# Kernel optimization log

Hardware: AMD Instinct MI355X
Metric: run time of the kernel (lower is better)

Reference implementation:

```python
import jax, jax.numpy as jnp
import numpy as np

B, DV, W, H = 128, 2048, 14, 14
S = W * H            # 196 spatial positions
DQ = 2048            # question vector dim
DA = 1200            # attention dim_v == dim_q == dim_mm (MLB elementwise fusion)
G = 4                # nb_glimpses
DH = 2048            # fusion dim_h (total); per-glimpse = DH // G
NANS = 3000


def setup_inputs() -> dict:
    key = jax.random.key(0)
    ks = jax.random.split(key, 16)
    s = 0.02
    return {
        "input_v": jax.random.normal(ks[0], (B, DV, W, H), jnp.float32),
        "x_q_vec": jax.random.normal(ks[1], (B, DQ), jnp.float32),
        # conv_v_att: 1x1 conv DV->DA  (expressed as channel matmul)
        "Wv_att": jax.random.normal(ks[2], (DV, DA), jnp.float32) * s,
        "bv_att": jnp.zeros((DA,), jnp.float32),
        # linear_q_att: DQ->DA
        "Wq_att": jax.random.normal(ks[3], (DQ, DA), jnp.float32) * s,
        "bq_att": jnp.zeros((DA,), jnp.float32),
        # conv_att: 1x1 conv DA->G
        "Wa": jax.random.normal(ks[4], (DA, G), jnp.float32) * s,
        "ba": jnp.zeros((G,), jnp.float32),
        # per-glimpse fusion linears DV -> DH//G, stacked over glimpses
        "Wf": jax.random.normal(ks[5], (G, DV, DH // G), jnp.float32) * s,
        "bf": jnp.zeros((G, DH // G), jnp.float32),
        # linear_q_fusion: DQ -> DH
        "Wqf": jax.random.normal(ks[6], (DQ, DH), jnp.float32) * s,
        "bqf": jnp.zeros((DH,), jnp.float32),
        # linear_classif: DH -> NANS
        "Wc": jax.random.normal(ks[7], (DH, NANS), jnp.float32) * s,
        "bc": jnp.zeros((NANS,), jnp.float32),
    }


def reference(input_v, x_q_vec, Wv_att, bv_att, Wq_att, bq_att, Wa, ba,
              Wf, bf, Wqf, bqf, Wc, bc):
    b = input_v.shape[0]
    v_flat = input_v.reshape(b, DV, S)                      # [B, DV, S]

    # --- attention scores ---
    # conv_v_att (1x1) + tanh -> [B, S, DA]
    x_v = jnp.tanh(jnp.einsum('bcs,cd->bsd', v_flat, Wv_att) + bv_att)
    # linear_q_att + tanh -> [B, DA], broadcast over spatial
    x_q = jnp.tanh(x_q_vec @ Wq_att + bq_att)
    # MLB fusion_att: elementwise multiply, then tanh (activation_mm)
    x_att = jnp.tanh(x_v * x_q[:, None, :])                 # [B, S, DA]
    scores = jnp.einsum('bsd,dg->bsg', x_att, Wa) + ba      # [B, S, G]
    att = jax.nn.softmax(scores, axis=1)                    # softmax over spatial

    # --- weighted pooling per glimpse ---
    v_att = jnp.einsum('bsg,bcs->bgc', att, v_flat)         # [B, G, DV]

    # --- fusion of glimpses ---
    xv = jnp.tanh(jnp.einsum('bgc,gch->bgh', v_att, Wf) + bf)  # [B, G, DH/G]
    xv = xv.reshape(b, DH)                                   # concat glimpses
    xq = jnp.tanh(x_q_vec @ Wqf + bqf)                       # [B, DH]
    x = xv * xq                                              # MLB fusion_classif

    # --- classifier ---
    x = jnp.tanh(x)
    return x @ Wc + bc                                       # [B, NANS]
```

## Files before the change

kernel.cpp:

```cpp
#include <hip/hip_runtime.h>
#include <hip/hip_bf16.h>

#define BB   128
#define DV   2048
#define SS   196
#define DQ   2048
#define DA   1200
#define DAP  1280
#define GG   4
#define DH   2048
#define NANS 3000
#define NANSP 3008
#define MROWS (BB*SS)
#define NT   10
#define KSPLIT 8
#define KCHUNK (DV/KSPLIT)
#define NQ   (DAP + DH)

typedef __attribute__((ext_vector_type(8))) short bf16x8;
typedef __attribute__((ext_vector_type(4))) float f32x4;

__device__ __forceinline__ float fast_tanh(float x) {
    float e = __expf(2.0f * x);
    return 1.0f - 2.0f * __builtin_amdgcn_rcpf(e + 1.0f);
}

__device__ __forceinline__ void async_copy16(const void* gsrc, void* ldst) {
    __builtin_amdgcn_global_load_lds(
        (const __attribute__((address_space(1))) void*)gsrc,
        (__attribute__((address_space(3))) void*)ldst, 16, 0, 0);
}

__global__ void pad_misc(const float* __restrict__ bv, const float* __restrict__ Wa,
                         float* __restrict__ bvp, float* __restrict__ wap) {
    int i = blockIdx.x * 256 + threadIdx.x;
    if (i < DAP) bvp[i] = (i < DA) ? bv[i] : 0.f;
    if (i < DAP * GG) {
        int d = i >> 2;
        wap[i] = (d < DA) ? Wa[i] : 0.f;
    }
}

__global__ __launch_bounds__(256) void transpose_v(const float* __restrict__ v,
                                                   __hip_bfloat16* __restrict__ vt) {
    __shared__ float tile[128][65];
    const int b  = blockIdx.z;
    const int c0 = blockIdx.x * 128;
    const int s0 = blockIdx.y * 64;
    const int t  = threadIdx.x;
    const int sl = t & 63;
    const int cr = t >> 6;
    const float* src = v + (size_t)b * DV * SS;
    const int sg = s0 + sl;
    const bool sok = sg < SS;
#pragma unroll
    for (int i = 0; i < 32; ++i) {
        int c = cr + i * 4;
        tile[c][sl] = sok ? src[(size_t)(c0 + c) * SS + sg] : 0.f;
    }
    __syncthreads();
    const int cp = (t & 63) * 2;
#pragma unroll
    for (int i = 0; i < 16; ++i) {
        int s = (t >> 6) + i * 4;
        int sgl = s0 + s;
        if (sgl < SS) {
            __hip_bfloat162 h2;
            h2.x = __float2bfloat16(tile[cp][s]);
            h2.y = __float2bfloat16(tile[cp + 1][s]);
            *(__hip_bfloat162*)(vt + ((size_t)b * SS + sgl) * DV + c0 + cp) = h2;
        }
    }
}

__global__ __launch_bounds__(256) void transpose_w(const float* __restrict__ Wv,
                                                   __hip_bfloat16* __restrict__ wvt) {
    __shared__ float tile[64][65];
    const int d0 = blockIdx.x * 64;
    const int c0 = blockIdx.y * 64;
    const int t  = threadIdx.x;
    const int col  = t & 63;
    const int rowb = t >> 6;
#pragma unroll
    for (int i = 0; i < 16; ++i) {
        int c = rowb + i * 4;
        int d = d0 + col;
        tile[c][col] = (d < DA) ? Wv[(size_t)(c0 + c) * DA + d] : 0.f;
    }
    __syncthreads();
#pragma unroll
    for (int i = 0; i < 16; ++i) {
        int dl = rowb + i * 4;
        wvt[(size_t)(d0 + dl) * DV + c0 + col] = __float2bfloat16(tile[col][dl]);
    }
}

template <int SEL>
__global__ __launch_bounds__(256) void gemm_partial(
    const float* __restrict__ A, int lda,
    const float* __restrict__ Bm, const float* __restrict__ B2,
    float* __restrict__ Cp, int Npad) {
    __shared__ float As[64 * 132];
    __shared__ float Bs[64 * 68];
    const int t     = threadIdx.x;
    const int n0    = blockIdx.x * 64;
    const int kbase = blockIdx.y * KCHUNK;

    const float* Aeff = A;
    const float* Beff;
    int ldb, ncol0, nlim;
    if (SEL == 0) {
        Beff = Bm; ldb = NANS; ncol0 = n0; nlim = NANS;
    } else if (SEL == 1) {
        int gg = n0 >> 9;
        Aeff = A + gg * 2048;
        Beff = Bm + (size_t)gg * 2048 * 512;
        ldb = 512; ncol0 = n0 & 511; nlim = 1 << 30;
    } else {
        if (n0 < DAP) { Beff = Bm; ldb = DA; ncol0 = n0;      nlim = DA; }
        else          { Beff = B2; ldb = DH; ncol0 = n0 - DAP; nlim = 1 << 30; }
    }

    const int tm = (t & 31) * 4;
    const int tn = (t >> 5) * 8;
    float acc[4][8] = {};

    for (int k0 = kbase; k0 < kbase + KCHUNK; k0 += 64) {
        {
            int kk = t & 63, mb = (t >> 6) * 32;
#pragma unroll
            for (int i = 0; i < 32; ++i)
                As[kk * 132 + mb + i] = Aeff[(size_t)(mb + i) * lda + k0 + kk];
        }
        {
            int j = t & 63, kr = t >> 6;
            bool ok = (ncol0 + j) < nlim;
#pragma unroll
            for (int i = 0; i < 16; ++i) {
                int k = kr + i * 4;
                Bs[k * 68 + j] = ok ? Beff[(size_t)(k0 + k) * ldb + ncol0 + j] : 0.f;
            }
        }
        __syncthreads();
#pragma unroll
        for (int kk = 0; kk < 64; ++kk) {
            const float4 av = *(const float4*)(As + kk * 132 + tm);
            const float4 b0 = *(const float4*)(Bs + kk * 68 + tn);
            const float4 b1 = *(const float4*)(Bs + kk * 68 + tn + 4);
            const float am[4] = {av.x, av.y, av.z, av.w};
#pragma unroll
            for (int i = 0; i < 4; ++i) {
                acc[i][0] += am[i] * b0.x; acc[i][1] += am[i] * b0.y;
                acc[i][2] += am[i] * b0.z; acc[i][3] += am[i] * b0.w;
                acc[i][4] += am[i] * b1.x; acc[i][5] += am[i] * b1.y;
                acc[i][6] += am[i] * b1.z; acc[i][7] += am[i] * b1.w;
            }
        }
        __syncthreads();
    }
#pragma unroll
    for (int i = 0; i < 4; ++i) {
        size_t base = ((size_t)blockIdx.y * 128 + tm + i) * Npad + n0 + tn;
        float4 v0 = {acc[i][0], acc[i][1], acc[i][2], acc[i][3]};
        float4 v1 = {acc[i][4], acc[i][5], acc[i][6], acc[i][7]};
        *(float4*)(Cp + base) = v0;
        *(float4*)(Cp + base + 4) = v1;
    }
}

template <int MODE>
__global__ __launch_bounds__(256) void gemm_epilogue(
    const float* __restrict__ Cp, int Npad, int Nreal,
    const float* __restrict__ bias, const float* __restrict__ aux,
    float* __restrict__ out, int ldo) {
    int n = blockIdx.x * 256 + threadIdx.x;
    int m = blockIdx.y;
    if (n >= Npad) return;
    float s = 0.f;
#pragma unroll
    for (int ks = 0; ks < KSPLIT; ++ks)
        s += Cp[((size_t)ks * 128 + m) * Npad + n];
    if (MODE == 0) {
        if (n >= Nreal) return;
        out[(size_t)m * ldo + n] = s + bias[n];
    } else {
        float xv = fast_tanh(s + bias[n]);
        out[(size_t)m * ldo + n] = fast_tanh(xv * aux[(size_t)m * 2048 + n]);
    }
}

__global__ __launch_bounds__(256) void epilogue_q(
    const float* __restrict__ Cp,
    const float* __restrict__ bqa, const float* __restrict__ bqf,
    float* __restrict__ qatt, float* __restrict__ qfus) {
    int n = blockIdx.x * 256 + threadIdx.x;
    int m = blockIdx.y;
    if (n >= NQ) return;
    float s = 0.f;
#pragma unroll
    for (int ks = 0; ks < KSPLIT; ++ks)
        s += Cp[((size_t)ks * 128 + m) * NQ + n];
    if (n < DAP) {
        qatt[(size_t)m * DAP + n] = (n < DA) ? fast_tanh(s + bqa[n]) : 0.f;
    } else {
        int j = n - DAP;
        qfus[(size_t)m * DH + j] = fast_tanh(s + bqf[j]);
    }
}

__global__ __launch_bounds__(256) void big_gemm(
    const __hip_bfloat16* __restrict__ vt,
    const __hip_bfloat16* __restrict__ wt,
    const float* __restrict__ bvp,
    const float* __restrict__ qatt,
    const float* __restrict__ wap,
    float* __restrict__ scores_p) {
    __shared__ __hip_bfloat16 As[128 * 64];
    __shared__ __hip_bfloat16 Bs[128 * 64];
    __shared__ float wa_s[128 * 4];
    __shared__ float sc[128 * 4];
    __shared__ float qs[2 * 128];
    const int t    = threadIdx.x;
    const int lane = t & 63;
    const int w    = t >> 6;
    const int wm   = w >> 1, wn = w & 1;

    int bid = blockIdx.x;
    int grp = bid / 80, r = bid % 80;
    int mt, nt;
    if (grp < 24) { mt = grp * 8 + (r & 7); nt = r >> 3; }
    else          { mt = 192 + (r & 3);     nt = r >> 2; }
    const int m0 = mt * 128, n0 = nt * 128;
    const int b0 = m0 / SS;
    const int b1 = (m0 + 127) / SS;
    const int bsplit = (b0 + 1) * SS;

    if (t < 128) {
        *(float4*)(wa_s + t * 4) = *(const float4*)(wap + (n0 + t) * 4);
        *(float4*)(sc + t * 4) = (float4){0.f, 0.f, 0.f, 0.f};
        qs[t]       = qatt[(size_t)b0 * DAP + n0 + t];
        qs[128 + t] = qatt[(size_t)b1 * DAP + n0 + t];
    }

    f32x4 acc[4][4];
#pragma unroll
    for (int i = 0; i < 4; ++i)
#pragma unroll
        for (int j = 0; j < 4; ++j) acc[i][j] = (f32x4){0.f, 0.f, 0.f, 0.f};

    const int srow   = lane >> 3;
    const int schunk = (lane & 7) ^ srow;
    const __hip_bfloat16* aG = vt + (size_t)(m0 + w * 32 + srow) * DV + schunk * 8;
    const __hip_bfloat16* bG = wt + (size_t)(n0 + w * 32 + srow) * DV + schunk * 8;
    __hip_bfloat16* aL = As + (w * 32) * 64;
    __hip_bfloat16* bL = Bs + (w * 32) * 64;

    for (int k0 = 0; k0 < DV; k0 += 64) {
        __syncthreads();
#pragma unroll
        for (int j = 0; j < 4; ++j) {
            async_copy16(aG + (size_t)(j * 8) * DV + k0, aL + j * 8 * 64);
            async_copy16(bG + (size_t)(j * 8) * DV + k0, bL + j * 8 * 64);
        }
        __syncthreads();
#pragma unroll
        for (int ks = 0; ks < 2; ++ks) {
            const int cx = ((ks * 4 + (lane >> 4)) ^ (lane & 7)) * 8;
            bf16x8 a[4], b[4];
#pragma unroll
            for (int mi = 0; mi < 4; ++mi)
                a[mi] = *(const bf16x8*)(As + (wm * 64 + mi * 16 + (lane & 15)) * 64 + cx);
#pragma unroll
            for (int ni = 0; ni < 4; ++ni)
                b[ni] = *(const bf16x8*)(Bs + (wn * 64 + ni * 16 + (lane & 15)) * 64 + cx);
#pragma unroll
            for (int mi = 0; mi < 4; ++mi)
#pragma unroll
                for (int ni = 0; ni < 4; ++ni)
                    acc[mi][ni] = __builtin_amdgcn_mfma_f32_16x16x32_bf16(a[mi], b[ni], acc[mi][ni], 0, 0, 0);
        }
    }

    const int colb_l = wn * 64 + (lane & 15);
    const int colb_g = n0 + colb_l;
    float bvv[4];
    float4 wv[4];
#pragma unroll
    for (int ni = 0; ni < 4; ++ni) {
        bvv[ni] = bvp[colb_g + ni * 16];
        wv[ni]  = *(const float4*)(wa_s + (colb_l + ni * 16) * 4);
    }
#pragma unroll
    for (int mi = 0; mi < 4; ++mi) {
#pragma unroll
        for (int rr = 0; rr < 4; ++rr) {
            int lrow = wm * 64 + mi * 16 + ((lane >> 4) << 2) + rr;
            int row  = m0 + lrow;
            int qoff = (row >= bsplit) ? 128 : 0;
            float p0 = 0.f, p1 = 0.f, p2 = 0.f, p3 = 0.f;
#pragma unroll
            for (int ni = 0; ni < 4; ++ni) {
                float xv = fast_tanh(acc[mi][ni][rr] + bvv[ni]);
                float xa = fast_tanh(xv * qs[qoff + colb_l + ni * 16]);
                p0 += xa * wv[ni].x; p1 += xa * wv[ni].y;
                p2 += xa * wv[ni].z; p3 += xa * wv[ni].w;
            }
#pragma unroll
            for (int mk = 1; mk < 16; mk <<= 1) {
                p0 += __shfl_xor(p0, mk); p1 += __shfl_xor(p1, mk);
                p2 += __shfl_xor(p2, mk); p3 += __shfl_xor(p3, mk);
            }
            if ((lane & 15) == 0) {
                atomicAdd(sc + lrow * 4 + 0, p0);
                atomicAdd(sc + lrow * 4 + 1, p1);
                atomicAdd(sc + lrow * 4 + 2, p2);
                atomicAdd(sc + lrow * 4 + 3, p3);
            }
        }
    }
    __syncthreads();
    if (t < 128)
        *(float4*)(scores_p + ((size_t)nt * MROWS + m0 + t) * 4) = *(float4*)(sc + t * 4);
}

__global__ __launch_bounds__(256) void softmax_pool(
    const float* __restrict__ scores_p,
    const __hip_bfloat16* __restrict__ vt,
    float* __restrict__ vatt) {
    __shared__ __align__(16) float att[SS * GG];
    const int b = blockIdx.y;
    const int t = threadIdx.x;
    if (t < SS) {
        float4 s = {0.f, 0.f, 0.f, 0.f};
#pragma unroll
        for (int ntile = 0; ntile < NT; ++ntile) {
            float4 p = *(const float4*)(scores_p + ((size_t)ntile * MROWS + b * SS + t) * 4);
            s.x += p.x; s.y += p.y; s.z += p.z; s.w += p.w;
        }
        *(float4*)(att + t * 4) = s;
    }
    __syncthreads();
    {
        const int g = t >> 6;
        const int lane = t & 63;
        float mx = -3.0e38f;
        for (int s = lane; s < SS; s += 64) mx = fmaxf(mx, att[s * 4 + g]);
#pragma unroll
        for (int m = 32; m > 0; m >>= 1) mx = fmaxf(mx, __shfl_xor(mx, m));
        float sum = 0.f;
        for (int s = lane; s < SS; s += 64) sum += __expf(att[s * 4 + g] - mx);
#pragma unroll
        for (int m = 32; m > 0; m >>= 1) sum += __shfl_xor(sum, m);
        float inv = __builtin_amdgcn_rcpf(sum);
        for (int s = lane; s < SS; s += 64) att[s * 4 + g] = __expf(att[s * 4 + g] - mx) * inv;
    }
    __syncthreads();
    const int c = blockIdx.x * 512 + t * 2;
    const __hip_bfloat16* vp = vt + (size_t)b * SS * DV + c;
    float a00 = 0, a01 = 0, a02 = 0, a03 = 0;
    float a10 = 0, a11 = 0, a12 = 0, a13 = 0;
#pragma unroll 4
    for (int s = 0; s < SS; ++s) {
        unsigned u = *(const unsigned*)(vp + (size_t)s * DV);
        float v0 = __uint_as_float(u << 16);
        float v1 = __uint_as_float(u & 0xffff0000u);
        float4 aw = *(const float4*)(att + s * 4);
        a00 += v0 * aw.x; a01 += v0 * aw.y; a02 += v0 * aw.z; a03 += v0 * aw.w;
        a10 += v1 * aw.x; a11 += v1 * aw.y; a12 += v1 * aw.z; a13 += v1 * aw.w;
    }
    float* vb = vatt + (size_t)b * GG * DV;
    vb[0 * DV + c] = a00; vb[0 * DV + c + 1] = a10;
    vb[1 * DV + c] = a01; vb[1 * DV + c + 1] = a11;
    vb[2 * DV + c] = a02; vb[2 * DV + c + 1] = a12;
    vb[3 * DV + c] = a03; vb[3 * DV + c + 1] = a13;
}

extern "C" void kernel_launch(void* const* d_in, const int* in_sizes, int n_in,
                              void* d_out, int out_size, void* d_ws, size_t ws_size,
                              hipStream_t stream) {
    const float* input_v = (const float*)d_in[0];
    const float* x_q     = (const float*)d_in[1];
    const float* Wv      = (const float*)d_in[2];
    const float* bv      = (const float*)d_in[3];
    const float* Wq_att  = (const float*)d_in[4];
    const float* bq_att  = (const float*)d_in[5];
    const float* Wa      = (const float*)d_in[6];
    const float* Wf      = (const float*)d_in[8];
    const float* bf_     = (const float*)d_in[9];
    const float* Wqf     = (const float*)d_in[10];
    const float* bqf     = (const float*)d_in[11];
    const float* Wc      = (const float*)d_in[12];
    const float* bc      = (const float*)d_in[13];
    float* out = (float*)d_out;

    char* wsb = (char*)d_ws;
    size_t off = 0;
    auto carve = [&](size_t bytes) -> void* {
        void* p = wsb + off;
        off += (bytes + 255) & ~(size_t)255;
        return p;
    };
    __hip_bfloat16* vt  = (__hip_bfloat16*)carve((size_t)MROWS * DV * 2);
    __hip_bfloat16* wvt = (__hip_bfloat16*)carve((size_t)DAP * DV * 2);
    float* Cp       = (float*)carve((size_t)KSPLIT * 128 * NQ * 4);
    float* scores_p = (float*)carve((size_t)NT * MROWS * GG * 4);
    float* qatt = (float*)carve((size_t)BB * DAP * 4);
    float* qfus = (float*)carve((size_t)BB * DH * 4);
    float* bvp  = (float*)carve((size_t)DAP * 4);
    float* wap  = (float*)carve((size_t)DAP * GG * 4);
    float* vatt = (float*)carve((size_t)BB * GG * DV * 4);
    float* xbuf = (float*)carve((size_t)BB * DH * 4);
    (void)ws_size; (void)n_in; (void)in_sizes; (void)out_size;

    pad_misc<<<dim3(20), 256, 0, stream>>>(bv, Wa, bvp, wap);
    transpose_v<<<dim3(DV / 128, 4, BB), 256, 0, stream>>>(input_v, vt);
    transpose_w<<<dim3(DAP / 64, DV / 64), 256, 0, stream>>>(Wv, wvt);

    gemm_partial<2><<<dim3(NQ / 64, KSPLIT), 256, 0, stream>>>(
        x_q, DQ, Wq_att, Wqf, Cp, NQ);
    epilogue_q<<<dim3(NQ / 256, BB), 256, 0, stream>>>(Cp, bq_att, bqf, qatt, qfus);

    big_gemm<<<dim3(24 * 80 + 40), 256, 0, stream>>>(vt, wvt, bvp, qatt, wap, scores_p);

    softmax_pool<<<dim3(4, BB), 256, 0, stream>>>(scores_p, vt, vatt);

    gemm_partial<1><<<dim3(DH / 64, KSPLIT), 256, 0, stream>>>(
        vatt, GG * DV, Wf, nullptr, Cp, DH);
    gemm_epilogue<2><<<dim3(DH / 256, BB), 256, 0, stream>>>(
        Cp, DH, DH, bf_, qfus, xbuf, DH);

    gemm_partial<0><<<dim3(NANSP / 64, KSPLIT), 256, 0, stream>>>(
        xbuf, DH, Wc, nullptr, Cp, NANSP);
    gemm_epilogue<0><<<dim3(NANSP / 256 + 1, BB), 256, 0, stream>>>(
        Cp, NANSP, NANS, bc, nullptr, out, NANS);
}
```

Baseline: 777.3 us.

## Move small GEMMs to bf16 MFMA split-K and load big_gemm B operand directly to registers

After: 879.2 us. +13.1%, slower.

```diff
diff --git a/kernel.cpp b/kernel.cpp
--- a/kernel.cpp
+++ b/kernel.cpp
@@ -10,12 +10,12 @@
 #define GG   4
 #define DH   2048
 #define NANS 3000
-#define NANSP 3008
+#define NANSP 3072
 #define MROWS (BB*SS)
 #define NT   10
-#define KSPLIT 8
-#define KCHUNK (DV/KSPLIT)
 #define NQ   (DAP + DH)
+#define KS2  16
+#define KCH2 (DV/KS2)
 
 typedef __attribute__((ext_vector_type(8))) short bf16x8;
 typedef __attribute__((ext_vector_type(4))) float f32x4;
@@ -31,9 +31,14 @@
         (__attribute__((address_space(3))) void*)ldst, 16, 0, 0);
 }
 
-__global__ void pad_misc(const float* __restrict__ bv, const float* __restrict__ Wa,
-                         float* __restrict__ bvp, float* __restrict__ wap) {
+__global__ __launch_bounds__(256) void prep(const float* __restrict__ x_q,
+                                            const float* __restrict__ bv,
+                                            const float* __restrict__ Wa,
+                                            __hip_bfloat16* __restrict__ xqb,
+                                            float* __restrict__ bvp,
+                                            float* __restrict__ wap) {
     int i = blockIdx.x * 256 + threadIdx.x;
+    if (i < BB * DQ) xqb[i] = __float2bfloat16(x_q[i]);
     if (i < DAP) bvp[i] = (i < DA) ? bv[i] : 0.f;
     if (i < DAP * GG) {
         int d = i >> 2;
@@ -73,10 +78,13 @@
     }
 }
 
-__global__ __launch_bounds__(256) void transpose_w(const float* __restrict__ Wv,
-                                                   __hip_bfloat16* __restrict__ wvt) {
+__global__ __launch_bounds__(256) void transpose_nk(
+    const float* __restrict__ src, int ldsrc, int nreal,
+    __hip_bfloat16* __restrict__ dst, size_t srcz, int dstzrows) {
+    src += (size_t)blockIdx.z * srcz;
+    dst += (size_t)blockIdx.z * dstzrows * 2048;
     __shared__ float tile[64][65];
-    const int d0 = blockIdx.x * 64;
+    const int n0 = blockIdx.x * 64;
     const int c0 = blockIdx.y * 64;
     const int t  = threadIdx.x;
     const int col  = t & 63;
@@ -84,109 +92,78 @@
 #pragma unroll
     for (int i = 0; i < 16; ++i) {
         int c = rowb + i * 4;
-        int d = d0 + col;
-        tile[c][col] = (d < DA) ? Wv[(size_t)(c0 + c) * DA + d] : 0.f;
+        int n = n0 + col;
+        tile[c][col] = (n < nreal) ? src[(size_t)(c0 + c) * ldsrc + n] : 0.f;
     }
     __syncthreads();
 #pragma unroll
     for (int i = 0; i < 16; ++i) {
-        int dl = rowb + i * 4;
-        wvt[(size_t)(d0 + dl) * DV + c0 + col] = __float2bfloat16(tile[col][dl]);
-    }
-}
-
-template <int SEL>
-__global__ __launch_bounds__(256) void gemm_partial(
-    const float* __restrict__ A, int lda,
-    const float* __restrict__ Bm, const float* __restrict__ B2,
-    float* __restrict__ Cp, int Npad) {
-    __shared__ float As[64 * 132];
-    __shared__ float Bs[64 * 68];
-    const int t     = threadIdx.x;
-    const int n0    = blockIdx.x * 64;
-    const int kbase = blockIdx.y * KCHUNK;
-
-    const float* Aeff = A;
-    const float* Beff;
-    int ldb, ncol0, nlim;
-    if (SEL == 0) {
-        Beff = Bm; ldb = NANS; ncol0 = n0; nlim = NANS;
-    } else if (SEL == 1) {
-        int gg = n0 >> 9;
-        Aeff = A + gg * 2048;
-        Beff = Bm + (size_t)gg * 2048 * 512;
-        ldb = 512; ncol0 = n0 & 511; nlim = 1 << 30;
-    } else {
-        if (n0 < DAP) { Beff = Bm; ldb = DA; ncol0 = n0;      nlim = DA; }
-        else          { Beff = B2; ldb = DH; ncol0 = n0 - DAP; nlim = 1 << 30; }
-    }
-
-    const int tm = (t & 31) * 4;
-    const int tn = (t >> 5) * 8;
-    float acc[4][8] = {};
-
-    for (int k0 = kbase; k0 < kbase + KCHUNK; k0 += 64) {
-        {
-            int kk = t & 63, mb = (t >> 6) * 32;
-#pragma unroll
-            for (int i = 0; i < 32; ++i)
-                As[kk * 132 + mb + i] = Aeff[(size_t)(mb + i) * lda + k0 + kk];
-        }
-        {
-            int j = t & 63, kr = t >> 6;
-            bool ok = (ncol0 + j) < nlim;
-#pragma unroll
-            for (int i = 0; i < 16; ++i) {
-                int k = kr + i * 4;
-                Bs[k * 68 + j] = ok ? Beff[(size_t)(k0 + k) * ldb + ncol0 + j] : 0.f;
-            }
-        }
+        int nl = rowb + i * 4;
+        dst[(size_t)(n0 + nl) * 2048 + c0 + col] = __float2bfloat16(tile[col][nl]);
+    }
+}
+
+__global__ __launch_bounds__(256) void mfma_partial(
+    const __hip_bfloat16* __restrict__ A, int lda,
+    const __hip_bfloat16* __restrict__ Bt,
+    float* __restrict__ Cp, int Npad, int fus) {
+    __shared__ __hip_bfloat16 As[128 * 64];
+    const int t    = threadIdx.x;
+    const int lane = t & 63;
+    const int w    = t >> 6;
+    const int wm   = w >> 1, wn = w & 1;
+    const int n0   = blockIdx.x * 128;
+    const int kbase = blockIdx.y * KCH2;
+    const __hip_bfloat16* Ae = A + (fus ? ((size_t)(n0 >> 9) * 2048) : 0);
+
+    f32x4 acc[4][4];
+#pragma unroll
+    for (int i = 0; i < 4; ++i)
+#pragma unroll
+        for (int j = 0; j < 4; ++j) acc[i][j] = (f32x4){0.f, 0.f, 0.f, 0.f};
+
+    const int srow   = lane >> 3;
+    const int schunk = (lane & 7) ^ srow;
+    const __hip_bfloat16* aG = Ae + (size_t)(w * 32 + srow) * lda + kbase + schunk * 8;
+    __hip_bfloat16* aL = As + (w * 32) * 64;
+    const __hip_bfloat16* bG =
+        Bt + (size_t)(n0 + wn * 64 + (lane & 15)) * 2048 + kbase + (lane >> 4) * 8;
+
+    for (int kk = 0; kk < KCH2; kk += 64) {
         __syncthreads();
 #pragma unroll
-        for (int kk = 0; kk < 64; ++kk) {
-            const float4 av = *(const float4*)(As + kk * 132 + tm);
-            const float4 b0 = *(const float4*)(Bs + kk * 68 + tn);
-            const float4 b1 = *(const float4*)(Bs + kk * 68 + tn + 4);
-            const float am[4] = {av.x, av.y, av.z, av.w};
-#pragma unroll
-            for (int i = 0; i < 4; ++i) {
-                acc[i][0] += am[i] * b0.x; acc[i][1] += am[i] * b0.y;
-                acc[i][2] += am[i] * b0.z; acc[i][3] += am[i] * b0.w;
-                acc[i][4] += am[i] * b1.x; acc[i][5] += am[i] * b1.y;
-                acc[i][6] += am[i] * b1.z; acc[i][7] += am[i] * b1.w;
-            }
-        }
+        for (int j = 0; j < 4; ++j)
+            async_copy16(aG + (size_t)(j * 8) * lda + kk, aL + j * 8 * 64);
+        bf16x8 b[2][4];
+#pragma unroll
+        for (int ks = 0; ks < 2; ++ks)
+#pragma unroll
+            for (int ni = 0; ni < 4; ++ni)
+                b[ks][ni] = *(const bf16x8*)(bG + (size_t)(ni * 16) * 2048 + kk + ks * 32);
         __syncthreads();
-    }
-#pragma unroll
-    for (int i = 0; i < 4; ++i) {
-        size_t base = ((size_t)blockIdx.y * 128 + tm + i) * Npad + n0 + tn;
-        float4 v0 = {acc[i][0], acc[i][1], acc[i][2], acc[i][3]};
-        float4 v1 = {acc[i][4], acc[i][5], acc[i][6], acc[i][7]};
-        *(float4*)(Cp + base) = v0;
-        *(float4*)(Cp + base + 4) = v1;
-    }
-}
-
-template <int MODE>
-__global__ __launch_bounds__(256) void gemm_epilogue(
-    const float* __restrict__ Cp, int Npad, int Nreal,
-    const float* __restrict__ bias, const float* __restrict__ aux,
-    float* __restrict__ out, int ldo) {
-    int n = blockIdx.x * 256 + threadIdx.x;
-    int m = blockIdx.y;
-    if (n >= Npad) return;
-    float s = 0.f;
-#pragma unroll
-    for (int ks = 0; ks < KSPLIT; ++ks)
-        s += Cp[((size_t)ks * 128 + m) * Npad + n];
-    if (MODE == 0) {
-        if (n >= Nreal) return;
-        out[(size_t)m * ldo + n] = s + bias[n];
-    } else {
-        float xv = fast_tanh(s + bias[n]);
-        out[(size_t)m * ldo + n] = fast_tanh(xv * aux[(size_t)m * 2048 + n]);
-    }
+#pragma unroll
+        for (int ks = 0; ks < 2; ++ks) {
+            const int cx = ((ks * 4 + (lane >> 4)) ^ (lane & 7)) * 8;
+            bf16x8 a[4];
+#pragma unroll
+            for (int mi = 0; mi < 4; ++mi)
+                a[mi] = *(const bf16x8*)(As + (wm * 64 + mi * 16 + (lane & 15)) * 64 + cx);
+#pragma unroll
+            for (int mi = 0; mi < 4; ++mi)
+#pragma unroll
+                for (int ni = 0; ni < 4; ++ni)
+                    acc[mi][ni] = __builtin_amdgcn_mfma_f32_16x16x32_bf16(a[mi], b[ks][ni], acc[mi][ni], 0, 0, 0);
+        }
+    }
+#pragma unroll
+    for (int mi = 0; mi < 4; ++mi)
+#pragma unroll
+        for (int r = 0; r < 4; ++r) {
+            int row = wm * 64 + mi * 16 + ((lane >> 4) << 2) + r;
+            float* cp = Cp + ((size_t)blockIdx.y * 128 + row) * Npad + n0 + wn * 64 + (lane & 15);
+#pragma unroll
+            for (int ni = 0; ni < 4; ++ni) cp[ni * 16] = acc[mi][ni][r];
+        }
 }
 
 __global__ __launch_bounds__(256) void epilogue_q(
@@ -198,13 +175,35 @@
     if (n >= NQ) return;
     float s = 0.f;
 #pragma unroll
-    for (int ks = 0; ks < KSPLIT; ++ks)
+    for (int ks = 0; ks < KS2; ++ks)
         s += Cp[((size_t)ks * 128 + m) * NQ + n];
     if (n < DAP) {
         qatt[(size_t)m * DAP + n] = (n < DA) ? fast_tanh(s + bqa[n]) : 0.f;
     } else {
         int j = n - DAP;
         qfus[(size_t)m * DH + j] = fast_tanh(s + bqf[j]);
+    }
+}
+
+template <int MODE>
+__global__ __launch_bounds__(256) void gemm_epilogue(
+    const float* __restrict__ Cp, int Npad, int Nreal,
+    const float* __restrict__ bias, const float* __restrict__ aux,
+    void* __restrict__ outv, int ldo) {
+    int n = blockIdx.x * 256 + threadIdx.x;
+    int m = blockIdx.y;
+    if (n >= Npad) return;
+    float s = 0.f;
+#pragma unroll
+    for (int ks = 0; ks < KS2; ++ks)
+        s += Cp[((size_t)ks * 128 + m) * Npad + n];
+    if (MODE == 0) {
+        if (n >= Nreal) return;
+        ((float*)outv)[(size_t)m * ldo + n] = s + bias[n];
+    } else {
+        float xv = fast_tanh(s + bias[n]);
+        float o  = fast_tanh(xv * aux[(size_t)m * 2048 + n]);
+        ((__hip_bfloat16*)outv)[(size_t)m * ldo + n] = __float2bfloat16(o);
     }
 }
 
@@ -216,7 +215,6 @@
     const float* __restrict__ wap,
     float* __restrict__ scores_p) {
     __shared__ __hip_bfloat16 As[128 * 64];
-    __shared__ __hip_bfloat16 Bs[128 * 64];
     __shared__ float wa_s[128 * 4];
     __shared__ float sc[128 * 4];
     __shared__ float qs[2 * 128];
@@ -251,33 +249,34 @@
     const int srow   = lane >> 3;
     const int schunk = (lane & 7) ^ srow;
     const __hip_bfloat16* aG = vt + (size_t)(m0 + w * 32 + srow) * DV + schunk * 8;
-    const __hip_bfloat16* bG = wt + (size_t)(n0 + w * 32 + srow) * DV + schunk * 8;
     __hip_bfloat16* aL = As + (w * 32) * 64;
-    __hip_bfloat16* bL = Bs + (w * 32) * 64;
+    const __hip_bfloat16* bG =
+        wt + (size_t)(n0 + wn * 64 + (lane & 15)) * DV + (lane >> 4) * 8;
 
     for (int k0 = 0; k0 < DV; k0 += 64) {
         __syncthreads();
 #pragma unroll
-        for (int j = 0; j < 4; ++j) {
+        for (int j = 0; j < 4; ++j)
             async_copy16(aG + (size_t)(j * 8) * DV + k0, aL + j * 8 * 64);
-            async_copy16(bG + (size_t)(j * 8) * DV + k0, bL + j * 8 * 64);
-        }
+        bf16x8 b[2][4];
+#pragma unroll
+        for (int ks = 0; ks < 2; ++ks)
+#pragma unroll
+            for (int ni = 0; ni < 4; ++ni)
+                b[ks][ni] = *(const bf16x8*)(bG + (size_t)(ni * 16) * DV + k0 + ks * 32);
         __syncthreads();
 #pragma unroll
         for (int ks = 0; ks < 2; ++ks) {
             const int cx = ((ks * 4 + (lane >> 4)) ^ (lane & 7)) * 8;
-            bf16x8 a[4], b[4];
+            bf16x8 a[4];
 #pragma unroll
             for (int mi = 0; mi < 4; ++mi)
                 a[mi] = *(const bf16x8*)(As + (wm * 64 + mi * 16 + (lane & 15)) * 64 + cx);
 #pragma unroll
-            for (int ni = 0; ni < 4; ++ni)
-                b[ni] = *(const bf16x8*)(Bs + (wn * 64 + ni * 16 + (lane & 15)) * 64 + cx);
-#pragma unroll
             for (int mi = 0; mi < 4; ++mi)
 #pragma unroll
                 for (int ni = 0; ni < 4; ++ni)
-                    acc[mi][ni] = __builtin_amdgcn_mfma_f32_16x16x32_bf16(a[mi], b[ni], acc[mi][ni], 0, 0, 0);
+                    acc[mi][ni] = __builtin_amdgcn_mfma_f32_16x16x32_bf16(a[mi], b[ks][ni], acc[mi][ni], 0, 0, 0);
         }
     }
 
@@ -326,7 +325,7 @@
 __global__ __launch_bounds__(256) void softmax_pool(
     const float* __restrict__ scores_p,
     const __hip_bfloat16* __restrict__ vt,
-    float* __restrict__ vatt) {
+    __hip_bfloat16* __restrict__ vattb) {
     __shared__ __align__(16) float att[SS * GG];
     const int b = blockIdx.y;
     const int t = threadIdx.x;
@@ -368,11 +367,16 @@
         a00 += v0 * aw.x; a01 += v0 * aw.y; a02 += v0 * aw.z; a03 += v0 * aw.w;
         a10 += v1 * aw.x; a11 += v1 * aw.y; a12 += v1 * aw.z; a13 += v1 * aw.w;
     }
-    float* vb = vatt + (size_t)b * GG * DV;
-    vb[0 * DV + c] = a00; vb[0 * DV + c + 1] = a10;
-    vb[1 * DV + c] = a01; vb[1 * DV + c + 1] = a11;
-    vb[2 * DV + c] = a02; vb[2 * DV + c + 1] = a12;
-    vb[3 * DV + c] = a03; vb[3 * DV + c + 1] = a13;
+    __hip_bfloat16* vb = vattb + (size_t)b * GG * DV;
+    __hip_bfloat162 h;
+    h.x = __float2bfloat16(a00); h.y = __float2bfloat16(a10);
+    *(__hip_bfloat162*)(vb + 0 * DV + c) = h;
+    h.x = __float2bfloat16(a01); h.y = __float2bfloat16(a11);
+    *(__hip_bfloat162*)(vb + 1 * DV + c) = h;
+    h.x = __float2bfloat16(a02); h.y = __float2bfloat16(a12);
+    *(__hip_bfloat162*)(vb + 2 * DV + c) = h;
+    h.x = __float2bfloat16(a03); h.y = __float2bfloat16(a13);
+    *(__hip_bfloat162*)(vb + 3 * DV + c) = h;
 }
 
 extern "C" void kernel_launch(void* const* d_in, const int* in_sizes, int n_in,
@@ -400,37 +404,41 @@
         off += (bytes + 255) & ~(size_t)255;
         return p;
     };
-    __hip_bfloat16* vt  = (__hip_bfloat16*)carve((size_t)MROWS * DV * 2);
-    __hip_bfloat16* wvt = (__hip_bfloat16*)carve((size_t)DAP * DV * 2);
-    float* Cp       = (float*)carve((size_t)KSPLIT * 128 * NQ * 4);
+    __hip_bfloat16* vt   = (__hip_bfloat16*)carve((size_t)MROWS * DV * 2);
+    __hip_bfloat16* wvt  = (__hip_bfloat16*)carve((size_t)DAP * DV * 2);
+    __hip_bfloat16* wqT  = (__hip_bfloat16*)carve((size_t)NQ * 2048 * 2);
+    __hip_bfloat16* wfT  = (__hip_bfloat16*)carve((size_t)DH * 2048 * 2);
+    float* Cp       = (float*)carve((size_t)KS2 * 128 * NQ * 4);
     float* scores_p = (float*)carve((size_t)NT * MROWS * GG * 4);
     float* qatt = (float*)carve((size_t)BB * DAP * 4);
     float* qfus = (float*)carve((size_t)BB * DH * 4);
     float* bvp  = (float*)carve((size_t)DAP * 4);
     float* wap  = (float*)carve((size_t)DAP * GG * 4);
-    float* vatt = (float*)carve((size_t)BB * GG * DV * 4);
-    float* xbuf = (float*)carve((size_t)BB * DH * 4);
+    __hip_bfloat16* xqb   = (__hip_bfloat16*)carve((size_t)BB * DQ * 2);
+    __hip_bfloat16* vattb = (__hip_bfloat16*)carve((size_t)BB * GG * DV * 2);
+    __hip_bfloat16* xbufb = (__hip_bfloat16*)carve((size_t)BB * DH * 2);
+    __hip_bfloat16* wcT = wqT;
     (void)ws_size; (void)n_in; (void)in_sizes; (void)out_size;
 
-    pad_misc<<<dim3(20), 256, 0, stream>>>(bv, Wa, bvp, wap);
+    prep<<<dim3((BB * DQ + 255) / 256), 256, 0, stream>>>(x_q, bv, Wa, xqb, bvp, wap);
     transpose_v<<<dim3(DV / 128, 4, BB), 256, 0, stream>>>(input_v, vt);
-    transpose_w<<<dim3(DAP / 64, DV / 64), 256, 0, stream>>>(Wv, wvt);
-
-    gemm_partial<2><<<dim3(NQ / 64, KSPLIT), 256, 0, stream>>>(
-        x_q, DQ, Wq_att, Wqf, Cp, NQ);
+    transpose_nk<<<dim3(DAP / 64, 32), 256, 0, stream>>>(Wv, DA, DA, wvt, 0, 0);
+    transpose_nk<<<dim3(DAP / 64, 32), 256, 0, stream>>>(Wq_att, DA, DA, wqT, 0, 0);
+    transpose_nk<<<dim3(DH / 64, 32), 256, 0, stream>>>(Wqf, DH, DH, wqT + (size_t)DAP * 2048, 0, 0);
+    transpose_nk<<<dim3(8, 32, 4), 256, 0, stream>>>(Wf, 512, 512, wfT, (size_t)2048 * 512, 512);
+
+    mfma_partial<<<dim3(NQ / 128, KS2), 256, 0, stream>>>(xqb, DQ, wqT, Cp, NQ, 0);
     epilogue_q<<<dim3(NQ / 256, BB), 256, 0, stream>>>(Cp, bq_att, bqf, qatt, qfus);
 
+    transpose_nk<<<dim3(NANSP / 64, 32), 256, 0, stream>>>(Wc, NANS, NANS, wcT, 0, 0);
+
     big_gemm<<<dim3(24 * 80 + 40), 256, 0, stream>>>(vt, wvt, bvp, qatt, wap, scores_p);
 
-    softmax_pool<<<dim3(4, BB), 256, 0, stream>>>(scores_p, vt, vatt);
-
-    gemm_partial<1><<<dim3(DH / 64, KSPLIT), 256, 0, stream>>>(
-        vatt, GG * DV, Wf, nullptr, Cp, DH);
-    gemm_epilogue<2><<<dim3(DH / 256, BB), 256, 0, stream>>>(
-        Cp, DH, DH, bf_, qfus, xbuf, DH);
-
-    gemm_partial<0><<<dim3(NANSP / 64, KSPLIT), 256, 0, stream>>>(
-        xbuf, DH, Wc, nullptr, Cp, NANSP);
-    gemm_epilogue<0><<<dim3(NANSP / 256 + 1, BB), 256, 0, stream>>>(
-        Cp, NANSP, NANS, bc, nullptr, out, NANS);
-}
+    softmax_pool<<<dim3(4, BB), 256, 0, stream>>>(scores_p, vt, vattb);
+
+    mfma_partial<<<dim3(DH / 128, KS2), 256, 0, stream>>>(vattb, GG * DV, wfT, Cp, DH, 1);
+    gemm_epilogue<2><<<dim3(DH / 256, BB), 256, 0, stream>>>(Cp, DH, DH, bf_, qfus, xbufb, DH);
+
+    mfma_partial<<<dim3(NANSP / 128, KS2), 256, 0, stream>>>(xbufb, DH, wcT, Cp, NANSP, 0);
+    gemm_epilogue<0><<<dim3(NANSP / 256, BB), 256, 0, stream>>>(Cp, NANSP, NANS, bc, nullptr, out, NANS);
+}
```
